# Kernel tuning notes

Hardware: AMD Instinct MI355X
Metric: run time of the kernel (lower is better)

Reference implementation:

```python
import jax, jax.numpy as jnp
import numpy as np

NUM_EMBEDDINGS = 1024
EMBEDDING_DIM = 256
COMMITMENT_COST = 0.02


def setup_inputs() -> dict:
    key = jax.random.key(0)
    k1, k2 = jax.random.split(key)
    z = jax.random.normal(k1, (64, 256, 32, 32), dtype=jnp.float32)
    # torch init: uniform(-1/K, 1/K)
    emb = jax.random.uniform(k2, (NUM_EMBEDDINGS, EMBEDDING_DIM), dtype=jnp.float32,
                             minval=-1.0 / NUM_EMBEDDINGS, maxval=1.0 / NUM_EMBEDDINGS)
    return {"z": z, "emb": emb}


def reference(z, emb):
    n, d, h, w = z.shape
    # (N, D, H, W) -> (N*H*W, D)
    z_flat = jnp.transpose(z, (0, 2, 3, 1)).reshape(-1, d)
    # squared L2 distances: ||z||^2 - 2 z.E^T + ||E||^2  -> (NHW, K)
    distances = (jnp.sum(z_flat * z_flat, axis=1, keepdims=True)
                 - 2.0 * z_flat @ emb.T
                 + jnp.sum(emb * emb, axis=1))
    indices = jnp.argmin(distances, axis=1)  # (NHW,)
    z_q = jnp.transpose(emb[indices].reshape(n, h, w, d), (0, 3, 1, 2))  # (N, D, H, W)
    # straight-through estimator
    z_q_st = z + jax.lax.stop_gradient(z_q - z)
    commitment_loss = COMMITMENT_COST * jnp.mean((jax.lax.stop_gradient(z) - z_q) ** 2)
    codebook_loss = jnp.mean((z - jax.lax.stop_gradient(z_q)) ** 2)
    vq_loss = commitment_loss + codebook_loss
    indices_reshaped = indices.reshape(n, h, w)
    return z_q_st, indices_reshaped, vq_loss
```

## Files before the change

### kernel.cpp

```cpp
#include <hip/hip_runtime.h>
#include <hip/hip_bf16.h>
#include <float.h>

#define OUT_IDX_OFF 16777216
#define OUT_LOSS_OFF 16842752
#define CAND_OFF 8388608
#define GMIN_OFF 12582912
#define GCNT_OFF 13107200
#define NSLOT 32
#define DELTA 2.0e-3f

typedef __attribute__((ext_vector_type(8))) short short8;
typedef __attribute__((ext_vector_type(4))) float f32x4;

static __device__ __forceinline__ unsigned short f2bf(float f) {
  union { __hip_bfloat16 h; unsigned short u; } cv;
  cv.h = __float2bfloat16(f);
  return cv.u;
}

__global__ __launch_bounds__(256) void k_prep(const float* __restrict__ emb,
                                              unsigned short* __restrict__ E2,
                                              float* __restrict__ cws) {
  const int k = blockIdx.x, d = threadIdx.x;
  const float v = emb[k * 256 + d];
  __shared__ float red[256];
  __shared__ unsigned short row[256];
  row[d] = f2bf(v);
  red[d] = v * v;
  __syncthreads();
  for (int s = 128; s > 0; s >>= 1) {
    if (d < s) red[d] += red[d + s];
    __syncthreads();
  }
  if (d == 0) cws[k] = red[0];
  if (d < 32) ((short8*)&E2[k * 256])[d] = ((short8*)row)[d];
}

__global__ __launch_bounds__(256) void k_cvt2(const float* __restrict__ z,
                                              unsigned short* __restrict__ A2) {
  __shared__ float tile[64][65];
  const int t = threadIdx.x;
  const int pt = blockIdx.x >> 2, dt = blockIdx.x & 3;
  const int p0 = pt << 6, d0 = dt << 6;
  const int n = p0 >> 10, hw0 = p0 & 1023;
  const float* zb = z + (size_t)n * 262144 + (size_t)d0 * 1024 + hw0;
  const int hwl = (t & 15) << 2;
#pragma unroll
  for (int i = 0; i < 4; ++i) {
    const int dl = (t >> 4) + i * 16;
    const float4 v = *(const float4*)&zb[(size_t)dl * 1024 + hwl];
    tile[hwl + 0][dl] = v.x;
    tile[hwl + 1][dl] = v.y;
    tile[hwl + 2][dl] = v.z;
    tile[hwl + 3][dl] = v.w;
  }
  __syncthreads();
  const int pl = t >> 2, c = t & 3;
  unsigned short* dst = &A2[(size_t)(p0 + pl) * 256 + d0];
#pragma unroll
  for (int h = 0; h < 2; ++h) {
    const int ch = c + h * 4;
    unsigned short tmp[8];
#pragma unroll
    for (int j = 0; j < 8; ++j) tmp[j] = f2bf(tile[pl][ch * 8 + j]);
    *(short8*)&dst[ch * 8] = *(short8*)tmp;
  }
}

__global__ __launch_bounds__(256) void k_a(const float* __restrict__ z,
                                           float* __restrict__ aws) {
#pragma clang fp contract(off)
  const int t = threadIdx.x;
  const int r = (blockIdx.x << 7) + (t & 127);
  const int h = t >> 7;
  const int n = r >> 10;
  const int hw = r & 1023;
  const float* zp = z + (size_t)n * 262144 + hw + (size_t)h * 131072;
  float acc[8];
#pragma unroll
  for (int j = 0; j < 8; ++j) {
    const float x = zp[(size_t)j * 1024];
    acc[j] = x * x;
  }
  for (int g = 1; g < 16; ++g) {
#pragma unroll
    for (int j = 0; j < 8; ++j) {
      const float x = zp[(size_t)(g * 8 + j) * 1024];
      const float p = x * x;
      acc[j] = acc[j] + p;
    }
  }
  const float s = ((acc[0] + acc[1]) + (acc[2] + acc[3])) +
                  ((acc[4] + acc[5]) + (acc[6] + acc[7]));
  __shared__ float red[256];
  red[t] = s;
  __syncthreads();
  if (t < 128) aws[(blockIdx.x << 7) + t] = red[t] + red[t + 128];
}

__global__ __launch_bounds__(256, 3) void k_gemm2(
    const unsigned short* __restrict__ A2, const unsigned short* __restrict__ E2,
    const float* __restrict__ cws, const float* __restrict__ aws,
    int* __restrict__ gmin, int* __restrict__ gcnt,
    float2* __restrict__ gcand) {
  __shared__ __align__(16) unsigned short As[128 * 64];
  __shared__ __align__(16) unsigned short Bs[128 * 64];
  __shared__ float a_l[128], c_l[128], rmkt[256], bmin[128];

  const int t = threadIdx.x;
  const int lane = t & 63, wave = t >> 6;
  const int wr = wave >> 1, wc = wave & 1;
  const int quad = lane >> 4, l15 = lane & 15;
  const int rb = blockIdx.x >> 3, ck = blockIdx.x & 7;
  const int r0 = rb << 7, k0 = ck << 7;

  if (t < 128) {
    a_l[t] = aws[r0 + t];
    c_l[t] = cws[k0 + t];
  }

  const short8* gA8 = (const short8*)A2;
  const short8* gE8 = (const short8*)E2;
  const int srow = t >> 3;
  const int sch = t & 7;
  const int swst = (sch ^ (srow & 7)) << 3;
  const int swa = l15 & 7;

  f32x4 acc[4][4];
#pragma unroll
  for (int a = 0; a < 4; ++a)
#pragma unroll
    for (int b = 0; b < 4; ++b) acc[a][b] = (f32x4)(0.0f);

  for (int kt = 0; kt < 4; ++kt) {
    if (kt) __syncthreads();
    short8 va[4], vb[4];
#pragma unroll
    for (int s = 0; s < 4; ++s) {
      const int row = s * 32 + srow;
      va[s] = gA8[(size_t)(r0 + row) * 32 + kt * 8 + sch];
      vb[s] = gE8[(size_t)(k0 + row) * 32 + kt * 8 + sch];
    }
#pragma unroll
    for (int s = 0; s < 4; ++s) {
      const int row = s * 32 + srow;
      *(short8*)&As[row * 64 + swst] = va[s];
      *(short8*)&Bs[row * 64 + swst] = vb[s];
    }
    __syncthreads();
#pragma unroll
    for (int ks = 0; ks < 2; ++ks) {
      short8 af[4], bf[4];
#pragma unroll
      for (int tr = 0; tr < 4; ++tr)
        af[tr] = *(const short8*)&As[(wr * 64 + tr * 16 + l15) * 64 +
                                     (((ks * 4 + quad) ^ swa) << 3)];
#pragma unroll
      for (int tc = 0; tc < 4; ++tc)
        bf[tc] = *(const short8*)&Bs[(wc * 64 + tc * 16 + l15) * 64 +
                                     (((ks * 4 + quad) ^ swa) << 3)];
#pragma unroll
      for (int tr = 0; tr < 4; ++tr)
#pragma unroll
        for (int tc = 0; tc < 4; ++tc)
          acc[tr][tc] = __builtin_amdgcn_mfma_f32_16x16x32_bf16(
              af[tr], bf[tc], acc[tr][tc], 0, 0, 0);
    }
  }

#pragma unroll
  for (int tr = 0; tr < 4; ++tr)
#pragma unroll
    for (int rg = 0; rg < 4; ++rg) {
      const int rloc = wr * 64 + tr * 16 + quad * 4 + rg;
      const float av = a_l[rloc];
      float mn = FLT_MAX;
#pragma unroll
      for (int tc = 0; tc < 4; ++tc) {
        const int cloc = wc * 64 + tc * 16 + l15;
        const float s = av + fmaf(-2.0f, acc[tr][tc][rg], c_l[cloc]);
        mn = fminf(mn, s);
      }
      mn = fminf(mn, __shfl_xor(mn, 1));
      mn = fminf(mn, __shfl_xor(mn, 2));
      mn = fminf(mn, __shfl_xor(mn, 4));
      mn = fminf(mn, __shfl_xor(mn, 8));
      if (l15 == 0) rmkt[rloc * 2 + wc] = mn;
    }
  __syncthreads();
  if (t < 128) {
    const float m = fminf(rmkt[t * 2], rmkt[t * 2 + 1]);
    const int old = atomicMin(&gmin[r0 + t], __float_as_int(m));
    bmin[t] = fminf(m, __int_as_float(old));
  }
  __syncthreads();
#pragma unroll
  for (int tr = 0; tr < 4; ++tr)
#pragma unroll
    for (int rg = 0; rg < 4; ++rg) {
      const int rloc = wr * 64 + tr * 16 + quad * 4 + rg;
      const float av = a_l[rloc];
      const float lim = bmin[rloc] + DELTA;
#pragma unroll
      for (int tc = 0; tc < 4; ++tc) {
        const int cloc = wc * 64 + tc * 16 + l15;
        const float s = av + fmaf(-2.0f, acc[tr][tc][rg], c_l[cloc]);
        if (s <= lim) {
          const int pos = atomicAdd(&gcnt[r0 + rloc], 1);
          if (pos < NSLOT)
            gcand[(size_t)(r0 + rloc) * NSLOT + pos] =
                make_float2(s, __int_as_float(k0 + cloc));
        }
      }
    }
}

__global__ __launch_bounds__(256) void k_finish(
    const float* __restrict__ z, const float* __restrict__ emb,
    const float* __restrict__ cws, const float* __restrict__ aws,
    const int* __restrict__ gmin, const int* __restrict__ gcnt,
    const float2* __restrict__ gcand, int* __restrict__ idxws,
    float* __restrict__ out) {
  const int tid = (blockIdx.x << 8) + threadIdx.x;
  const int r = tid >> 2, sub = tid & 3;
  const float lim = __int_as_float(gmin[r]) + DELTA;
  int m = gcnt[r];
  if (m > NSLOT) m = NSLOT;
  const int n = r >> 10, hw = r & 1023;
  const float* zp = z + (size_t)n * 262144 + hw;
  const float a = aws[r];
  float bestv = FLT_MAX;
  int besti = 0x7fffffff;
  for (int ci = sub; ci < m; ci += 4) {
    const float2 p = gcand[(size_t)r * NSLOT + ci];
    if (p.x > lim) continue;
    const int k = __float_as_int(p.y);
    const float* ep = emb + (size_t)k * 256;
    float dot = 0.0f;
#pragma unroll 8
    for (int d = 0; d < 256; ++d) dot = fmaf(zp[(size_t)d * 1024], ep[d], dot);
    float s = fmaf(-2.0f, dot, a);
    s = s + cws[k];
    if (s < bestv || (s == bestv && k < besti)) {
      bestv = s;
      besti = k;
    }
  }
#pragma unroll
  for (int off = 1; off < 4; off <<= 1) {
    const float ov = __shfl_xor(bestv, off);
    const int oi = __shfl_xor(besti, off);
    if (ov < bestv || (ov == bestv && oi < besti)) {
      bestv = ov;
      besti = oi;
    }
  }
  if (sub == 0) {
    idxws[r] = besti;
    out[OUT_IDX_OFF + r] = (float)besti;
  }
  float c = (sub == 0) ? bestv : 0.0f;
#pragma unroll
  for (int off = 1; off < 64; off <<= 1) c += __shfl_xor(c, off);
  if ((threadIdx.x & 63) == 0)
    atomicAdd(&out[OUT_LOSS_OFF], c * (1.02f / 16777216.0f));
}

__global__ __launch_bounds__(256) void k_out2(const float* __restrict__ emb,
                                              const int* __restrict__ idxws,
                                              float* __restrict__ out) {
  __shared__ float zq[32][257];
  __shared__ int sidx[32];
  const int t = threadIdx.x;
  const int p0 = blockIdx.x << 5;
  const int n = p0 >> 10, hw0 = p0 & 1023;
  if (t < 32) sidx[t] = idxws[p0 + t];
  __syncthreads();
#pragma unroll
  for (int it = 0; it < 8; ++it) {
    const int i = t + (it << 8);
    const int p = i >> 6;
    const int q = (i & 63) << 2;
    const float4 v = *(const float4*)&emb[(size_t)sidx[p] * 256 + q];
    zq[p][q] = v.x;
    zq[p][q + 1] = v.y;
    zq[p][q + 2] = v.z;
    zq[p][q + 3] = v.w;
  }
  __syncthreads();
  const int p = t & 31, d0 = t >> 5;
  float* ob = out + (size_t)n * 262144 + hw0 + p;
#pragma unroll
  for (int dd = 0; dd < 32; ++dd) {
    const int d = (dd << 3) + d0;
    ob[(size_t)d * 1024] = zq[p][d];
  }
}

extern "C" void kernel_launch(void* const* d_in, const int* in_sizes, int n_in,
                              void* d_out, int out_size, void* d_ws,
                              size_t ws_size, hipStream_t stream) {
  const float* z = (const float*)d_in[0];
  const float* emb = (const float*)d_in[1];
  float* out = (float*)d_out;

  unsigned short* E2 = (unsigned short*)d_ws;
  float* cws = (float*)(E2 + 262144);
  float* aws = cws + 1024;
  int* idxws = (int*)(aws + 65536);
  unsigned short* A2 = (unsigned short*)d_out;
  float2* gcand = (float2*)(out + CAND_OFF);
  int* gmin = (int*)(out + GMIN_OFF);
  int* gcnt = (int*)(out + GCNT_OFF);

  hipMemsetAsync((char*)d_out + (size_t)OUT_LOSS_OFF * 4, 0, 4, stream);
  hipMemsetAsync(gmin, 0x7f, 65536 * 4, stream);
  hipMemsetAsync(gcnt, 0, 65536 * 4, stream);

  k_prep<<<dim3(1024), dim3(256), 0, stream>>>(emb, E2, cws);
  k_cvt2<<<dim3(4096), dim3(256), 0, stream>>>(z, A2);
  k_a<<<dim3(512), dim3(256), 0, stream>>>(z, aws);
  k_gemm2<<<dim3(4096), dim3(256), 0, stream>>>(A2, E2, cws, aws, gmin, gcnt,
                                                gcand);
  k_finish<<<dim3(1024), dim3(256), 0, stream>>>(z, emb, cws, aws, gmin, gcnt,
                                                 gcand, idxws, out);
  k_out2<<<dim3(2048), dim3(256), 0, stream>>>(emb, idxws, out);
}
```

Before: 337.8 us.

## Keep A tile in registers and stream full codebook per 64-row block

Replaces the 128x128 output-tile GEMM with one block per 64 rows that keeps its A fragments in registers and loops over all 1024 codebook entries. B tiles are double-buffered in LDS through direct global-to-LDS loads. The running minimum and candidate counts move into shared memory, which removes the global atomics and the two memsets. This cuts re-reading of A and global atomic traffic. In exchange it launches a quarter as many blocks, uses more registers, and does a barrier-heavy epilogue per codebook chunk.

```diff
diff --git a/kernel.cpp b/kernel.cpp
--- a/kernel.cpp
+++ b/kernel.cpp
@@ -99,121 +99,171 @@
   if (t < 128) aws[(blockIdx.x << 7) + t] = red[t] + red[t + 128];
 }
 
-__global__ __launch_bounds__(256, 3) void k_gemm2(
+__global__ __launch_bounds__(256, 3) void k_gemm3(
     const unsigned short* __restrict__ A2, const unsigned short* __restrict__ E2,
     const float* __restrict__ cws, const float* __restrict__ aws,
     int* __restrict__ gmin, int* __restrict__ gcnt,
     float2* __restrict__ gcand) {
-  __shared__ __align__(16) unsigned short As[128 * 64];
-  __shared__ __align__(16) unsigned short Bs[128 * 64];
-  __shared__ float a_l[128], c_l[128], rmkt[256], bmin[128];
+  __shared__ __align__(16) unsigned short Bs[2][8192];
+  __shared__ float c_all[1024];
+  __shared__ float a_l[64];
+  __shared__ float rmin_s[64];
+  __shared__ int rcnt_s[64];
+  __shared__ float rmkt[128];
 
   const int t = threadIdx.x;
-  const int lane = t & 63, wave = t >> 6;
-  const int wr = wave >> 1, wc = wave & 1;
+  const int lane = t & 63;
+  const int wv = __builtin_amdgcn_readfirstlane(t >> 6);
+  const int wr = wv >> 1, wc = wv & 1;
   const int quad = lane >> 4, l15 = lane & 15;
-  const int rb = blockIdx.x >> 3, ck = blockIdx.x & 7;
-  const int r0 = rb << 7, k0 = ck << 7;
-
-  if (t < 128) {
+  const int sw7 = l15 & 7;
+  const int r0 = blockIdx.x << 6;
+
+  unsigned short* As = &Bs[0][0];
+
+#pragma unroll
+  for (int i = 0; i < 8; ++i) {
+    const int blk = (wv << 3) + i;
+    const int L = (blk << 6) + lane;
+    const int row = L >> 5, gpos = L & 31;
+    const int gsrc = (gpos & 24) | ((gpos & 7) ^ (row & 7));
+    const unsigned short* src = A2 + (((size_t)(r0 + row)) << 8) + (gsrc << 3);
+    __builtin_amdgcn_global_load_lds(
+        (const __attribute__((address_space(1))) void*)src,
+        (__attribute__((address_space(3))) void*)(As + (blk << 9)), 16, 0, 0);
+  }
+  ((f32x4*)c_all)[t] = ((const f32x4*)cws)[t];
+  if (t < 64) {
     a_l[t] = aws[r0 + t];
-    c_l[t] = cws[k0 + t];
-  }
-
-  const short8* gA8 = (const short8*)A2;
-  const short8* gE8 = (const short8*)E2;
-  const int srow = t >> 3;
-  const int sch = t & 7;
-  const int swst = (sch ^ (srow & 7)) << 3;
-  const int swa = l15 & 7;
-
-  f32x4 acc[4][4];
-#pragma unroll
-  for (int a = 0; a < 4; ++a)
+    rmin_s[t] = FLT_MAX;
+    rcnt_s[t] = 0;
+  }
+  __syncthreads();
+
+  short8 af[16];
+#pragma unroll
+  for (int tr = 0; tr < 2; ++tr)
+#pragma unroll
+    for (int kst = 0; kst < 8; ++kst) {
+      const int rr = (wr << 5) + (tr << 4) + l15;
+      const int g = (kst << 2) + quad;
+      const int gphys = (g & 24) | ((g & 7) ^ (rr & 7));
+      af[tr * 8 + kst] = *(const short8*)&As[rr * 256 + (gphys << 3)];
+    }
+  __syncthreads();
+
+  int bdst[4], bsrc[4];
+#pragma unroll
+  for (int i = 0; i < 4; ++i) {
+    const int blk = (wv << 2) + i;
+    const int L = (blk << 6) + lane;
+    const int col = L >> 3, gpos = L & 7;
+    bdst[i] = blk << 9;
+    bsrc[i] = (col << 8) + ((gpos ^ (col & 7)) << 3);
+  }
+
+  auto stageB = [&](unsigned short* dst, int k0s, int kts) {
+#pragma unroll
+    for (int i = 0; i < 4; ++i) {
+      const unsigned short* src = E2 + (k0s << 8) + bsrc[i] + (kts << 6);
+      __builtin_amdgcn_global_load_lds(
+          (const __attribute__((address_space(1))) void*)src,
+          (__attribute__((address_space(3))) void*)(dst + bdst[i]), 16, 0, 0);
+    }
+  };
+
+  f32x4 acc[2][4];
+#pragma unroll
+  for (int a = 0; a < 2; ++a)
 #pragma unroll
     for (int b = 0; b < 4; ++b) acc[a][b] = (f32x4)(0.0f);
 
-  for (int kt = 0; kt < 4; ++kt) {
-    if (kt) __syncthreads();
-    short8 va[4], vb[4];
-#pragma unroll
-    for (int s = 0; s < 4; ++s) {
-      const int row = s * 32 + srow;
-      va[s] = gA8[(size_t)(r0 + row) * 32 + kt * 8 + sch];
-      vb[s] = gE8[(size_t)(k0 + row) * 32 + kt * 8 + sch];
-    }
-#pragma unroll
-    for (int s = 0; s < 4; ++s) {
-      const int row = s * 32 + srow;
-      *(short8*)&As[row * 64 + swst] = va[s];
-      *(short8*)&Bs[row * 64 + swst] = vb[s];
-    }
-    __syncthreads();
-#pragma unroll
-    for (int ks = 0; ks < 2; ++ks) {
-      short8 af[4], bf[4];
-#pragma unroll
-      for (int tr = 0; tr < 4; ++tr)
-        af[tr] = *(const short8*)&As[(wr * 64 + tr * 16 + l15) * 64 +
-                                     (((ks * 4 + quad) ^ swa) << 3)];
-#pragma unroll
-      for (int tc = 0; tc < 4; ++tc)
-        bf[tc] = *(const short8*)&Bs[(wc * 64 + tc * 16 + l15) * 64 +
-                                     (((ks * 4 + quad) ^ swa) << 3)];
-#pragma unroll
-      for (int tr = 0; tr < 4; ++tr)
-#pragma unroll
-        for (int tc = 0; tc < 4; ++tc)
-          acc[tr][tc] = __builtin_amdgcn_mfma_f32_16x16x32_bf16(
-              af[tr], bf[tc], acc[tr][tc], 0, 0, 0);
-    }
-  }
-
-#pragma unroll
-  for (int tr = 0; tr < 4; ++tr)
-#pragma unroll
-    for (int rg = 0; rg < 4; ++rg) {
-      const int rloc = wr * 64 + tr * 16 + quad * 4 + rg;
-      const float av = a_l[rloc];
-      float mn = FLT_MAX;
-#pragma unroll
-      for (int tc = 0; tc < 4; ++tc) {
-        const int cloc = wc * 64 + tc * 16 + l15;
-        const float s = av + fmaf(-2.0f, acc[tr][tc][rg], c_l[cloc]);
-        mn = fminf(mn, s);
+  stageB(&Bs[0][0], 0, 0);
+  __syncthreads();
+
+  for (int ck = 0; ck < 8; ++ck) {
+    const int k0 = ck << 7;
+#pragma unroll
+    for (int kt = 0; kt < 4; ++kt) {
+      if (kt < 3)
+        stageB(&Bs[(kt + 1) & 1][0], k0, kt + 1);
+      else if (ck < 7)
+        stageB(&Bs[0][0], k0 + 128, 0);
+
+      const unsigned short* bs = &Bs[kt & 1][0];
+#pragma unroll
+      for (int ks = 0; ks < 2; ++ks) {
+        short8 bfr[4];
+#pragma unroll
+        for (int tc = 0; tc < 4; ++tc) {
+          const int col = (wc << 6) + (tc << 4) + l15;
+          const int gphys = ((ks << 2) + quad) ^ sw7;
+          bfr[tc] = *(const short8*)&bs[col * 64 + (gphys << 3)];
+        }
+#pragma unroll
+        for (int tr = 0; tr < 2; ++tr)
+#pragma unroll
+          for (int tc = 0; tc < 4; ++tc)
+            acc[tr][tc] = __builtin_amdgcn_mfma_f32_16x16x32_bf16(
+                af[tr * 8 + kt * 2 + ks], bfr[tc], acc[tr][tc], 0, 0, 0);
       }
-      mn = fminf(mn, __shfl_xor(mn, 1));
-      mn = fminf(mn, __shfl_xor(mn, 2));
-      mn = fminf(mn, __shfl_xor(mn, 4));
-      mn = fminf(mn, __shfl_xor(mn, 8));
-      if (l15 == 0) rmkt[rloc * 2 + wc] = mn;
-    }
-  __syncthreads();
-  if (t < 128) {
-    const float m = fminf(rmkt[t * 2], rmkt[t * 2 + 1]);
-    const int old = atomicMin(&gmin[r0 + t], __float_as_int(m));
-    bmin[t] = fminf(m, __int_as_float(old));
-  }
-  __syncthreads();
-#pragma unroll
-  for (int tr = 0; tr < 4; ++tr)
-#pragma unroll
-    for (int rg = 0; rg < 4; ++rg) {
-      const int rloc = wr * 64 + tr * 16 + quad * 4 + rg;
-      const float av = a_l[rloc];
-      const float lim = bmin[rloc] + DELTA;
-#pragma unroll
-      for (int tc = 0; tc < 4; ++tc) {
-        const int cloc = wc * 64 + tc * 16 + l15;
-        const float s = av + fmaf(-2.0f, acc[tr][tc][rg], c_l[cloc]);
-        if (s <= lim) {
-          const int pos = atomicAdd(&gcnt[r0 + rloc], 1);
-          if (pos < NSLOT)
-            gcand[(size_t)(r0 + rloc) * NSLOT + pos] =
-                make_float2(s, __int_as_float(k0 + cloc));
-        }
+
+      if (kt == 3) {
+#pragma unroll
+        for (int tr = 0; tr < 2; ++tr)
+#pragma unroll
+          for (int rg = 0; rg < 4; ++rg) {
+            const int rloc = (wr << 5) + (tr << 4) + (quad << 2) + rg;
+            const float av = a_l[rloc];
+            float mn = FLT_MAX;
+#pragma unroll
+            for (int tc = 0; tc < 4; ++tc) {
+              const int k = k0 + (wc << 6) + (tc << 4) + l15;
+              const float s = av + fmaf(-2.0f, acc[tr][tc][rg], c_all[k]);
+              mn = fminf(mn, s);
+            }
+            mn = fminf(mn, __shfl_xor(mn, 1));
+            mn = fminf(mn, __shfl_xor(mn, 2));
+            mn = fminf(mn, __shfl_xor(mn, 4));
+            mn = fminf(mn, __shfl_xor(mn, 8));
+            if (l15 == 0) rmkt[rloc * 2 + wc] = mn;
+          }
+        __syncthreads();
+        if (t < 64)
+          rmin_s[t] = fminf(rmin_s[t], fminf(rmkt[t * 2], rmkt[t * 2 + 1]));
+        __syncthreads();
+#pragma unroll
+        for (int tr = 0; tr < 2; ++tr)
+#pragma unroll
+          for (int rg = 0; rg < 4; ++rg) {
+            const int rloc = (wr << 5) + (tr << 4) + (quad << 2) + rg;
+            const float av = a_l[rloc];
+            const float lim = rmin_s[rloc] + DELTA;
+#pragma unroll
+            for (int tc = 0; tc < 4; ++tc) {
+              const int k = k0 + (wc << 6) + (tc << 4) + l15;
+              const float s = av + fmaf(-2.0f, acc[tr][tc][rg], c_all[k]);
+              if (s <= lim) {
+                const int pos = atomicAdd(&rcnt_s[rloc], 1);
+                if (pos < NSLOT)
+                  gcand[(size_t)(r0 + rloc) * NSLOT + pos] =
+                      make_float2(s, __int_as_float(k));
+              }
+            }
+          }
+#pragma unroll
+        for (int a = 0; a < 2; ++a)
+#pragma unroll
+          for (int b = 0; b < 4; ++b) acc[a][b] = (f32x4)(0.0f);
       }
-    }
+      __syncthreads();
+    }
+  }
+
+  if (t < 64) {
+    gmin[r0 + t] = __float_as_int(rmin_s[t]);
+    gcnt[r0 + t] = rcnt_s[t];
+  }
 }
 
 __global__ __launch_bounds__(256) void k_finish(
@@ -315,13 +365,11 @@
   int* gcnt = (int*)(out + GCNT_OFF);
 
   hipMemsetAsync((char*)d_out + (size_t)OUT_LOSS_OFF * 4, 0, 4, stream);
-  hipMemsetAsync(gmin, 0x7f, 65536 * 4, stream);
-  hipMemsetAsync(gcnt, 0, 65536 * 4, stream);
 
   k_prep<<<dim3(1024), dim3(256), 0, stream>>>(emb, E2, cws);
   k_cvt2<<<dim3(4096), dim3(256), 0, stream>>>(z, A2);
   k_a<<<dim3(512), dim3(256), 0, stream>>>(z, aws);
-  k_gemm2<<<dim3(4096), dim3(256), 0, stream>>>(A2, E2, cws, aws, gmin, gcnt,
+  k_gemm3<<<dim3(1024), dim3(256), 0, stream>>>(A2, E2, cws, aws, gmin, gcnt,
                                                 gcand);
   k_finish<<<dim3(1024), dim3(256), 0, stream>>>(z, emb, cws, aws, gmin, gcnt,
                                                  gcand, idxws, out);
```

New measurement: 364.3 us. +7.8%, slower.

## Load GEMM tiles directly into LDS and remap block order for codebook reuse

Applied to the files above, without the earlier changes.

Replaces the register-staged global-to-shared copies in the distance GEMM with direct global_load_lds transfers. The swizzle moves to the source address so the existing swizzled LDS reads still work. Occupancy hint rises from 3 to 4 blocks per CU, and the block index is remapped so consecutive blocks share a codebook chunk across row tiles. The aims are fewer VGPRs, less copy latency and better cache locality, at the risk of wrong LDS placement if the per-wave layout assumption is off.

```diff
diff --git a/kernel.cpp b/kernel.cpp
--- a/kernel.cpp
+++ b/kernel.cpp
@@ -99,7 +99,7 @@
   if (t < 128) aws[(blockIdx.x << 7) + t] = red[t] + red[t + 128];
 }
 
-__global__ __launch_bounds__(256, 3) void k_gemm2(
+__global__ __launch_bounds__(256, 4) void k_gemm4(
     const unsigned short* __restrict__ A2, const unsigned short* __restrict__ E2,
     const float* __restrict__ cws, const float* __restrict__ aws,
     int* __restrict__ gmin, int* __restrict__ gcnt,
@@ -109,10 +109,15 @@
   __shared__ float a_l[128], c_l[128], rmkt[256], bmin[128];
 
   const int t = threadIdx.x;
-  const int lane = t & 63, wave = t >> 6;
+  const int lane = t & 63;
+  const int wave = __builtin_amdgcn_readfirstlane(t >> 6);
   const int wr = wave >> 1, wc = wave & 1;
   const int quad = lane >> 4, l15 = lane & 15;
-  const int rb = blockIdx.x >> 3, ck = blockIdx.x & 7;
+  const int swa = l15 & 7;
+
+  const int bid = blockIdx.x;
+  const int L = ((bid & 7) << 9) + (bid >> 3);
+  const int rb = L >> 3, ck = L & 7;
   const int r0 = rb << 7, k0 = ck << 7;
 
   if (t < 128) {
@@ -120,12 +125,8 @@
     c_l[t] = cws[k0 + t];
   }
 
-  const short8* gA8 = (const short8*)A2;
-  const short8* gE8 = (const short8*)E2;
   const int srow = t >> 3;
-  const int sch = t & 7;
-  const int swst = (sch ^ (srow & 7)) << 3;
-  const int swa = l15 & 7;
+  const int gpos = t & 7;
 
   f32x4 acc[4][4];
 #pragma unroll
@@ -135,18 +136,24 @@
 
   for (int kt = 0; kt < 4; ++kt) {
     if (kt) __syncthreads();
-    short8 va[4], vb[4];
-#pragma unroll
-    for (int s = 0; s < 4; ++s) {
-      const int row = s * 32 + srow;
-      va[s] = gA8[(size_t)(r0 + row) * 32 + kt * 8 + sch];
-      vb[s] = gE8[(size_t)(k0 + row) * 32 + kt * 8 + sch];
-    }
-#pragma unroll
-    for (int s = 0; s < 4; ++s) {
-      const int row = s * 32 + srow;
-      *(short8*)&As[row * 64 + swst] = va[s];
-      *(short8*)&Bs[row * 64 + swst] = vb[s];
+#pragma unroll
+    for (int i = 0; i < 4; ++i) {
+      const int row = (i << 5) + srow;
+      const int gsrc = gpos ^ (row & 7);
+      const unsigned short* sa =
+          A2 + (((size_t)(r0 + row)) << 8) + (kt << 6) + (gsrc << 3);
+      __builtin_amdgcn_global_load_lds(
+          (const __attribute__((address_space(1))) void*)sa,
+          (__attribute__((address_space(3))) void*)(As + (i << 11) +
+                                                    (wave << 9)),
+          16, 0, 0);
+      const unsigned short* sb =
+          E2 + (((size_t)(k0 + row)) << 8) + (kt << 6) + (gsrc << 3);
+      __builtin_amdgcn_global_load_lds(
+          (const __attribute__((address_space(1))) void*)sb,
+          (__attribute__((address_space(3))) void*)(Bs + (i << 11) +
+                                                    (wave << 9)),
+          16, 0, 0);
     }
     __syncthreads();
 #pragma unroll
@@ -321,7 +328,7 @@
   k_prep<<<dim3(1024), dim3(256), 0, stream>>>(emb, E2, cws);
   k_cvt2<<<dim3(4096), dim3(256), 0, stream>>>(z, A2);
   k_a<<<dim3(512), dim3(256), 0, stream>>>(z, aws);
-  k_gemm2<<<dim3(4096), dim3(256), 0, stream>>>(A2, E2, cws, aws, gmin, gcnt,
+  k_gemm4<<<dim3(4096), dim3(256), 0, stream>>>(A2, E2, cws, aws, gmin, gcnt,
                                                 gcand);
   k_finish<<<dim3(1024), dim3(256), 0, stream>>>(z, emb, cws, aws, gmin, gcnt,
                                                  gcand, idxws, out);
```

Result: faster. 317.9 us (-5.9%).
